# Performance work log

Hardware: AMD Instinct MI355X
Metric: run time of the kernel (lower is better)

Reference implementation:

```python
import jax, jax.numpy as jnp
import numpy as np

S, T, B = 32, 48, 1024      # src_len, tgt_len, batch
E, H = 256, 1024            # embedding, hidden
VS, VT = 256, 256           # source/target vocab


def setup_inputs() -> dict:
    key = jax.random.key(0)
    ks = jax.random.split(key, 20)
    s = 0.02
    n = jax.random.normal
    inp = {
        "src": jax.random.randint(ks[0], (S, B), 0, VS),
        "tgt": jax.random.randint(ks[1], (T, B), 0, VT),
        "enc_emb": n(ks[2], (VS, E), jnp.float32) * s,
        "enc_Wih0": n(ks[3], (4 * H, E), jnp.float32) * s,
        "enc_Whh0": n(ks[4], (4 * H, H), jnp.float32) * s,
        "enc_b0": jnp.zeros((4 * H,), jnp.float32),
        "enc_Wih1": n(ks[5], (4 * H, H), jnp.float32) * s,
        "enc_Whh1": n(ks[6], (4 * H, H), jnp.float32) * s,
        "enc_b1": jnp.zeros((4 * H,), jnp.float32),
        "dec_emb": n(ks[7], (VT, E), jnp.float32) * s,
        "dec_Wih0": n(ks[8], (4 * H, E), jnp.float32) * s,
        "dec_Whh0": n(ks[9], (4 * H, H), jnp.float32) * s,
        "dec_b0": jnp.zeros((4 * H,), jnp.float32),
        "dec_Wih1": n(ks[10], (4 * H, H), jnp.float32) * s,
        "dec_Whh1": n(ks[11], (4 * H, H), jnp.float32) * s,
        "dec_b1": jnp.zeros((4 * H,), jnp.float32),
        "fc_W": n(ks[12], (H, VT), jnp.float32) * s,
        "fc_b": jnp.zeros((VT,), jnp.float32),
    }
    return inp


def lstm_step(x, h, c, Wih, Whh, b):
    # PyTorch gate order: i, f, g, o
    z = x @ Wih.T + h @ Whh.T + b
    i, f, g, o = jnp.split(z, 4, axis=-1)
    c = jax.nn.sigmoid(f) * c + jax.nn.sigmoid(i) * jnp.tanh(g)
    h = jax.nn.sigmoid(o) * jnp.tanh(c)
    return h, c


def run_layer(xs, Wih, Whh, b):
    # xs: [S, B, in]; returns all hidden states and final (h, c)
    bsz = xs.shape[1]
    h0 = jnp.zeros((bsz, Whh.shape[1]), xs.dtype)

    def step(carry, x):
        h, c = lstm_step(x, carry[0], carry[1], Wih, Whh, b)
        return (h, c), h

    (h, c), hs = jax.lax.scan(step, (h0, h0), xs)
    return hs, h, c


def reference(src, tgt, enc_emb, enc_Wih0, enc_Whh0, enc_b0, enc_Wih1, enc_Whh1,
              enc_b1, dec_emb, dec_Wih0, dec_Whh0, dec_b0, dec_Wih1, dec_Whh1,
              dec_b1, fc_W, fc_b):
    # ---- Encoder: 2-layer LSTM over source ----
    xe = enc_emb[src]                                   # [S, B, E]
    hs0, h0, c0 = run_layer(xe, enc_Wih0, enc_Whh0, enc_b0)
    _, h1, c1 = run_layer(hs0, enc_Wih1, enc_Whh1, enc_b1)

    # ---- Decoder: per-timestep loop, teacher forcing ratio = 1.0 ----
    def dec_step(carry, tok):
        dh0, dc0, dh1, dc1 = carry
        x = dec_emb[tok]                                # [B, E]
        dh0, dc0 = lstm_step(x, dh0, dc0, dec_Wih0, dec_Whh0, dec_b0)
        dh1, dc1 = lstm_step(dh0, dh1, dc1, dec_Wih1, dec_Whh1, dec_b1)
        logits = dh1 @ fc_W + fc_b                      # [B, VT]
        return (dh0, dc0, dh1, dc1), logits

    _, logits = jax.lax.scan(dec_step, (h0, c0, h1, c1), tgt[:-1])  # [T-1, B, VT]
    # outputs[0] is never written in the original -> stays zeros
    out = jnp.concatenate([jnp.zeros((1,) + logits.shape[1:], logits.dtype), logits], axis=0)
    return out
```

## Files before the change

kernel.cpp:

```cpp
#include <hip/hip_runtime.h>
#include <hip/hip_fp16.h>

typedef __attribute__((ext_vector_type(8))) short short8;
typedef __attribute__((ext_vector_type(4))) float floatx4;

#define DEVFN static __device__ __forceinline__

DEVFN short f2h(float v) { return __half_as_short(__float2half(v)); }

DEVFN void gload16(const void* g, void* l) {
  void* gnc = const_cast<void*>(g);
  __builtin_amdgcn_global_load_lds(
      (__attribute__((address_space(1))) void*)gnc,
      (__attribute__((address_space(3))) void*)l, 16, 0, 0);
}

DEVFN unsigned* fset(unsigned* f, int role, int s, int gy) {
  return f + ((((role * 79) + s) * 8 + gy) << 5);
}

__global__ __launch_bounds__(256, 2) void pers_kernel(
    short* xe0, short* xe1, short* xd0, short* xd1,
    const short* wc_e0, const short* wc_e1, const short* wc_d0, const short* wc_d1,
    const float* eb0, const float* eb1, const float* db0, const float* db1,
    const short* embe, const short* embd,
    const int* __restrict__ src, const int* __restrict__ tgt,
    short* dh1, unsigned* flags) {
  __shared__ short smem[32768];
  const int tid = threadIdx.x;
  const int lane = tid & 63;
  const int wv = tid >> 6;
  const int wm = wv >> 1;
  const int wu = wv & 1;
  const int l15 = lane & 15;
  const int l4 = lane >> 4;
  const int bx = blockIdx.x;
  const int role1 = bx >> 5;
  const int ut = bx & 31;
  const int u0 = ut * 32;
  const int gy = blockIdx.y;
  const int m0 = gy * 128;
  const int srow = lane >> 3;
  const int swseg = ((lane & 7) * 16) ^ (srow * 16);
  const long SL0 = 1024l * 1280, SL1 = 1024l * 2048;

  float cst[16];
#pragma unroll
  for (int i = 0; i < 16; ++i) cst[i] = 0.f;

  for (int s = 0; s < 79; ++s) {
    unsigned* WA = nullptr;
    unsigned* WB = nullptr;
    if (!role1) {
      if (s >= 1) WA = fset(flags, 0, s - 1, gy);
      if (s >= 2) WB = fset(flags, 1, s - 2, gy);
    } else {
      WA = fset(flags, 0, s, gy);
      if (s >= 1) WB = fset(flags, 1, s - 1, gy);
    }
    if (WA || WB) {
      if (tid < 64) {
        unsigned* p = (tid < 32) ? (WA ? WA + tid : nullptr)
                                 : (WB ? WB + (tid - 32) : nullptr);
        if (p) {
          while (__hip_atomic_load(p, __ATOMIC_RELAXED,
                                   __HIP_MEMORY_SCOPE_AGENT) == 0u)
            __builtin_amdgcn_s_sleep(1);
          (void)__hip_atomic_load(p, __ATOMIC_ACQUIRE, __HIP_MEMORY_SCOPE_AGENT);
        }
      }
      __syncthreads();
    }

    const int enc = (s < 32) ? 1 : 0;
    const int t = enc ? s : s - 32;
    const int cur = t & 1, nxt = cur ^ 1;
    const short* A; const short* Wt; const float* bs; int ktot;
    short *d1 = nullptr, *d2 = nullptr, *d3 = nullptr, *xq = nullptr;
    int s1 = 0, o1 = 0, xs = 0;
    const short* xe = nullptr; const int* tk = nullptr;
    if (!role1) {
      if (enc) {
        A = xe0 + cur * SL0; Wt = wc_e0; bs = eb0; ktot = 1280;
        d2 = xe1 + cur * SL1;
        s1 = 1280; o1 = 256; xs = 1280;
        if (t < 31) { d1 = xe0 + nxt * SL0; xq = d1; xe = embe; tk = src + (t + 1) * 1024; }
        else        { d1 = xd0;             xq = xd0; xe = embd; tk = tgt; }
      } else {
        A = xd0 + cur * SL0; Wt = wc_d0; bs = db0; ktot = 1280;
        d1 = xd0 + nxt * SL0; s1 = 1280; o1 = 256;
        d2 = xd1 + cur * SL1;
        if (t < 46) { xq = xd0 + nxt * SL0; xs = 1280; xe = embd; tk = tgt + (t + 1) * 1024; }
      }
    } else {
      if (enc) {
        A = xe1 + cur * SL1; Wt = wc_e1; bs = eb1; ktot = 2048;
        d1 = (t < 31) ? (xe1 + nxt * SL1) : xd1; s1 = 2048; o1 = 1024;
      } else {
        A = xd1 + cur * SL1; Wt = wc_d1; bs = db1; ktot = 2048;
        d1 = xd1 + nxt * SL1; s1 = 2048; o1 = 1024;
        d3 = dh1 + (long)t * 1024 * 1024;
      }
    }

    floatx4 acc[4][4];
#pragma unroll
    for (int g = 0; g < 4; ++g)
#pragma unroll
      for (int mi = 0; mi < 4; ++mi) acc[g][mi] = (floatx4){0.f, 0.f, 0.f, 0.f};

    const char* Ab = (const char*)A;
    const char* Wb = (const char*)Wt;
    const long kbytes = (long)ktot * 2;
    const int nkb = ktot >> 6;

    auto stage = [&](int kb, int bufi) {
      const long kboff = (long)kb * 128;
      short* sb = smem + bufi * 16384;
#pragma unroll
      for (int ci = 0; ci < 8; ++ci) {
        const int c = wv * 8 + ci;
        void* lds = (void*)(sb + c * 512);
        if (c < 16) {
          const int row = c * 8 + srow;
          gload16(Ab + (long)(m0 + row) * kbytes + kboff + swseg, lds);
        } else {
          const int cb = c - 16;
          const int wrow = (cb >> 2) * 1024 + u0 + (cb & 3) * 8 + srow;
          gload16(Wb + (long)wrow * kbytes + kboff + swseg, lds);
        }
      }
    };

    stage(0, 0);
    __syncthreads();
    int buf = 0;
    for (int kb = 0; kb < nkb; ++kb) {
      if (kb + 1 < nkb) stage(kb + 1, buf ^ 1);
      const short* sb = smem + buf * 16384;
#pragma unroll
      for (int k0 = 0; k0 < 64; k0 += 32) {
        short8 fa[4];
        short8 fb[4];
#pragma unroll
        for (int mi = 0; mi < 4; ++mi) {
          const int r = wm * 64 + mi * 16 + l15;
          fa[mi] = *(const short8*)(sb + r * 64 + ((k0 + l4 * 8) ^ ((r & 7) << 3)));
        }
        {
          const int r = wu * 16 + l15;
          const int kk = (k0 + l4 * 8) ^ ((r & 7) << 3);
#pragma unroll
          for (int g = 0; g < 4; ++g)
            fb[g] = *(const short8*)(sb + 8192 + (g * 32 + r) * 64 + kk);
        }
#pragma unroll
        for (int g = 0; g < 4; ++g)
#pragma unroll
          for (int mi = 0; mi < 4; ++mi)
            asm volatile("v_mfma_f32_16x16x32_f16 %0, %1, %2, %0"
                         : "+v"(acc[g][mi])
                         : "v"(fa[mi]), "v"(fb[g]));
      }
      __syncthreads();
      buf ^= 1;
    }
    asm volatile("s_nop 7\ns_nop 7\ns_nop 7");

    const int u = u0 + wu * 16 + l15;
    const float bi = bs[u];
    const float bf_ = bs[1024 + u];
    const float bg = bs[2048 + u];
    const float bo = bs[3072 + u];
    short* ht = smem;
    const int uloc = wu * 16 + l15;
#pragma unroll
    for (int mi = 0; mi < 4; ++mi) {
#pragma unroll
      for (int j = 0; j < 4; ++j) {
        const float zi = acc[0][mi][j] + bi;
        const float zf = acc[1][mi][j] + bf_;
        const float zg = acc[2][mi][j] + bg;
        const float zo = acc[3][mi][j] + bo;
        const float gi = 1.f / (1.f + expf(-zi));
        const float gf = 1.f / (1.f + expf(-zf));
        const float gg = tanhf(zg);
        const float go = 1.f / (1.f + expf(-zo));
        const float cn = gf * cst[mi * 4 + j] + gi * gg;
        cst[mi * 4 + j] = cn;
        const int rl = wm * 64 + mi * 16 + l4 * 4 + j;
        ht[rl * 40 + uloc] = f2h(go * tanhf(cn));
      }
    }
    __syncthreads();

    {
      const int rl = tid >> 1;
      const int seg = (tid & 1) * 16;
      const short8 v0 = *(const short8*)(ht + rl * 40 + seg);
      const short8 v1 = *(const short8*)(ht + rl * 40 + seg + 8);
      const long col = u0 + seg;
      if (d1) {
        short* p = d1 + (long)(m0 + rl) * s1 + o1 + col;
        *(short8*)p = v0; *(short8*)(p + 8) = v1;
      }
      if (d2) {
        short* p = d2 + (long)(m0 + rl) * 2048 + col;
        *(short8*)p = v0; *(short8*)(p + 8) = v1;
      }
      if (d3) {
        short* p = d3 + (long)(m0 + rl) * 1024 + col;
        *(short8*)p = v0; *(short8*)(p + 8) = v1;
      }
    }
    if (xq && tid < 128) {
      const int i = ut * 128 + tid;
      const int row = i >> 5;
      const int e8 = (i & 31) * 8;
      const int b = m0 + row;
      const int tok = tk[b];
      const short8 v = *(const short8*)(xe + (long)tok * 256 + e8);
      *(short8*)(xq + (long)b * xs + e8) = v;
    }

    __syncthreads();
    if (tid == 0)
      __hip_atomic_store(fset(flags, role1, s, gy) + ut, 1u,
                         __ATOMIC_RELEASE, __HIP_MEMORY_SCOPE_AGENT);
  }
}

__global__ __launch_bounds__(256) void fc_kernel(
    const short* __restrict__ A, const short* __restrict__ W,
    const float* __restrict__ bias, float* __restrict__ outp) {
  __shared__ short smem[32768];
  const int tid = threadIdx.x;
  const int lane = tid & 63;
  const int wv = tid >> 6;
  const int wm = wv >> 1;
  const int wu = wv & 1;
  const int l15 = lane & 15;
  const int l4 = lane >> 4;
  const int u0 = blockIdx.x * 128;
  const int m0 = blockIdx.y * 128;
  const int srow = lane >> 3;
  const int swseg = ((lane & 7) * 16) ^ (srow * 16);

  floatx4 acc[4][4];
#pragma unroll
  for (int g = 0; g < 4; ++g)
#pragma unroll
    for (int mi = 0; mi < 4; ++mi) acc[g][mi] = (floatx4){0.f, 0.f, 0.f, 0.f};

  const char* Ab = (const char*)A;
  const char* Wb = (const char*)W;
  const long kbytes = 2048;
  const int nkb = 16;

  auto stage = [&](int kb, int bufi) {
    const long kboff = (long)kb * 128;
    short* sb = smem + bufi * 16384;
#pragma unroll
    for (int ci = 0; ci < 8; ++ci) {
      const int c = wv * 8 + ci;
      void* lds = (void*)(sb + c * 512);
      if (c < 16) {
        const int row = c * 8 + srow;
        gload16(Ab + (long)(m0 + row) * kbytes + kboff + swseg, lds);
      } else {
        const int cb = c - 16;
        const int wrow = (cb >> 2) * 32 + u0 + (cb & 3) * 8 + srow;
        gload16(Wb + (long)wrow * kbytes + kboff + swseg, lds);
      }
    }
  };

  stage(0, 0);
  __syncthreads();
  int buf = 0;
  for (int kb = 0; kb < nkb; ++kb) {
    if (kb + 1 < nkb) stage(kb + 1, buf ^ 1);
    const short* sb = smem + buf * 16384;
#pragma unroll
    for (int k0 = 0; k0 < 64; k0 += 32) {
      short8 fa[4];
      short8 fb[4];
#pragma unroll
      for (int mi = 0; mi < 4; ++mi) {
        const int r = wm * 64 + mi * 16 + l15;
        fa[mi] = *(const short8*)(sb + r * 64 + ((k0 + l4 * 8) ^ ((r & 7) << 3)));
      }
      {
        const int r = wu * 16 + l15;
        const int kk = (k0 + l4 * 8) ^ ((r & 7) << 3);
#pragma unroll
        for (int g = 0; g < 4; ++g)
          fb[g] = *(const short8*)(sb + 8192 + (g * 32 + r) * 64 + kk);
      }
#pragma unroll
      for (int g = 0; g < 4; ++g)
#pragma unroll
        for (int mi = 0; mi < 4; ++mi)
          asm volatile("v_mfma_f32_16x16x32_f16 %0, %1, %2, %0"
                       : "+v"(acc[g][mi])
                       : "v"(fa[mi]), "v"(fb[g]));
    }
    __syncthreads();
    buf ^= 1;
  }
  asm volatile("s_nop 7\ns_nop 7\ns_nop 7");

#pragma unroll
  for (int g = 0; g < 4; ++g) {
    const int n = u0 + g * 32 + wu * 16 + l15;
    const float bb = bias[n];
#pragma unroll
    for (int mi = 0; mi < 4; ++mi) {
#pragma unroll
      for (int j = 0; j < 4; ++j) {
        const int r = m0 + wm * 64 + mi * 16 + l4 * 4 + j;
        outp[(long)r * 256 + n] = acc[g][mi][j] + bb;
      }
    }
  }
}

__global__ void wprep(const float* __restrict__ A, const float* __restrict__ B,
                      short* __restrict__ dst, int N, int Ka, int Kb) {
  const int ktot = Ka + Kb;
  const int n8 = ktot >> 3;
  const int total = N * n8;
  for (int idx = blockIdx.x * 256 + threadIdx.x; idx < total; idx += gridDim.x * 256) {
    const int n = idx / n8;
    const int k = (idx - n * n8) * 8;
    const float* s = (k < Ka) ? (A + (long)n * Ka + k) : (B + (long)n * Kb + (k - Ka));
    short8 v;
#pragma unroll
    for (int j = 0; j < 8; ++j) v[j] = f2h(s[j]);
    *(short8*)(dst + (long)n * ktot + k) = v;
  }
}

__global__ void embprep(const float* __restrict__ s, short* __restrict__ d, int total8) {
  const int idx = blockIdx.x * 256 + threadIdx.x;
  if (idx >= total8) return;
  short8 v;
#pragma unroll
  for (int j = 0; j < 8; ++j) v[j] = f2h(s[idx * 8 + j]);
  *(short8*)(d + idx * 8) = v;
}

__global__ void fcwprep(const float* __restrict__ fcW, short* __restrict__ dst) {
  const int idx = blockIdx.x * 256 + threadIdx.x;
  const int v = idx & 255;
  const int h = (idx >> 8) * 8;
  short8 o;
#pragma unroll
  for (int j = 0; j < 8; ++j) o[j] = f2h(fcW[(long)(h + j) * 256 + v]);
  *(short8*)(dst + (long)v * 1024 + h) = o;
}

__global__ void initk(const int* __restrict__ src, const float* __restrict__ emb,
                      short* __restrict__ xe0, short* __restrict__ xe1) {
  const int idx = blockIdx.x * 256 + threadIdx.x;
  if (idx < 1024 * 160) {
    const int b = idx / 160;
    const int k = (idx - b * 160) * 8;
    short8 v;
    if (k < 256) {
      const int tok = src[b];
#pragma unroll
      for (int j = 0; j < 8; ++j) v[j] = f2h(emb[(long)tok * 256 + k + j]);
    } else {
#pragma unroll
      for (int j = 0; j < 8; ++j) v[j] = 0;
    }
    *(short8*)(xe0 + (long)b * 1280 + k) = v;
  } else {
    const int i = idx - 1024 * 160;
    if (i < 1024 * 128) {
      const int b = i >> 7;
      const int k = 1024 + (i & 127) * 8;
      short8 v;
#pragma unroll
      for (int j = 0; j < 8; ++j) v[j] = 0;
      *(short8*)(xe1 + (long)b * 2048 + k) = v;
    }
  }
}

extern "C" void kernel_launch(void* const* d_in, const int* in_sizes, int n_in,
                              void* d_out, int out_size, void* d_ws, size_t ws_size,
                              hipStream_t stream) {
  (void)in_sizes; (void)n_in; (void)out_size; (void)ws_size;
  const int* src = (const int*)d_in[0];
  const int* tgt = (const int*)d_in[1];
  const float* enc_emb = (const float*)d_in[2];
  const float* eW0i = (const float*)d_in[3];
  const float* eW0h = (const float*)d_in[4];
  const float* eb0 = (const float*)d_in[5];
  const float* eW1i = (const float*)d_in[6];
  const float* eW1h = (const float*)d_in[7];
  const float* eb1 = (const float*)d_in[8];
  const float* dec_emb = (const float*)d_in[9];
  const float* dW0i = (const float*)d_in[10];
  const float* dW0h = (const float*)d_in[11];
  const float* db0 = (const float*)d_in[12];
  const float* dW1i = (const float*)d_in[13];
  const float* dW1h = (const float*)d_in[14];
  const float* db1 = (const float*)d_in[15];
  const float* fcW = (const float*)d_in[16];
  const float* fcb = (const float*)d_in[17];
  float* out = (float*)d_out;

  char* ws = (char*)d_ws;
  size_t off = 0;
  auto carve = [&](size_t bytes) {
    void* p = ws + off;
    off += (bytes + 255) & ~(size_t)255;
    return p;
  };
  short* wc_e0 = (short*)carve(4096l * 1280 * 2);
  short* wc_e1 = (short*)carve(4096l * 2048 * 2);
  short* wc_d0 = (short*)carve(4096l * 1280 * 2);
  short* wc_d1 = (short*)carve(4096l * 2048 * 2);
  short* fcwt = (short*)carve(256l * 1024 * 2);
  short* embe = (short*)carve(256l * 256 * 2);
  short* embd = (short*)carve(256l * 256 * 2);
  short* xe0 = (short*)carve(2l * 1024 * 1280 * 2);
  short* xe1 = (short*)carve(2l * 1024 * 2048 * 2);
  short* xd0 = (short*)carve(2l * 1024 * 1280 * 2);
  short* xd1 = (short*)carve(2l * 1024 * 2048 * 2);
  short* dh1 = (short*)carve(47l * 1024 * 1024 * 2);
  const size_t flagbytes = 2l * 79 * 8 * 32 * 4;
  unsigned* flags = (unsigned*)carve(flagbytes);

  hipMemsetAsync(flags, 0, flagbytes, stream);
  hipMemsetAsync(out, 0, 1024l * 256 * 4, stream);

  wprep<<<2560, 256, 0, stream>>>(eW0i, eW0h, wc_e0, 4096, 256, 1024);
  wprep<<<4096, 256, 0, stream>>>(eW1i, eW1h, wc_e1, 4096, 1024, 1024);
  wprep<<<2560, 256, 0, stream>>>(dW0i, dW0h, wc_d0, 4096, 256, 1024);
  wprep<<<4096, 256, 0, stream>>>(dW1i, dW1h, wc_d1, 4096, 1024, 1024);
  embprep<<<32, 256, 0, stream>>>(enc_emb, embe, 8192);
  embprep<<<32, 256, 0, stream>>>(dec_emb, embd, 8192);
  fcwprep<<<128, 256, 0, stream>>>(fcW, fcwt);
  initk<<<1152, 256, 0, stream>>>(src, enc_emb, xe0, xe1);

  pers_kernel<<<dim3(64, 8), 256, 0, stream>>>(
      xe0, xe1, xd0, xd1, wc_e0, wc_e1, wc_d0, wc_d1,
      eb0, eb1, db0, db1, embe, embd, src, tgt, dh1, flags);

  fc_kernel<<<dim3(2, 376), 256, 0, stream>>>(dh1, fcwt, fcb, out + 1024l * 256);
}
```

Baseline: 4.210 ms.

## Deepen GEMM k-loop pipeline to 4-stage ring with k-tile of 32

Replaces the double-buffered 64-wide k-tile staging with a four-buffer ring of 32-wide k-tiles, keeping three tiles of global-to-LDS loads in flight via explicit vmcnt waits and a single barrier per iteration. The swizzle and row mapping are adjusted to the narrower tile. The aim is to hide global memory latency inside each recurrent step's GEMM. In exchange the loop runs twice as many iterations with one barrier each, so barrier and instruction overhead per MFMA rises.

```diff
diff --git a/kernel.cpp b/kernel.cpp
--- a/kernel.cpp
+++ b/kernel.cpp
@@ -40,8 +40,8 @@
   const int u0 = ut * 32;
   const int gy = blockIdx.y;
   const int m0 = gy * 128;
-  const int srow = lane >> 3;
-  const int swseg = ((lane & 7) * 16) ^ (srow * 16);
+  const int srow = lane >> 2;
+  const int sswz = ((lane & 3) * 16) ^ ((srow & 3) << 4);
   const long SL0 = 1024l * 1280, SL1 = 1024l * 2048;
 
   float cst[16];
@@ -112,59 +112,60 @@
     const char* Ab = (const char*)A;
     const char* Wb = (const char*)Wt;
     const long kbytes = (long)ktot * 2;
-    const int nkb = ktot >> 6;
+    const int nkb = ktot >> 5;
 
     auto stage = [&](int kb, int bufi) {
-      const long kboff = (long)kb * 128;
-      short* sb = smem + bufi * 16384;
-#pragma unroll
-      for (int ci = 0; ci < 8; ++ci) {
-        const int c = wv * 8 + ci;
-        void* lds = (void*)(sb + c * 512);
-        if (c < 16) {
-          const int row = c * 8 + srow;
-          gload16(Ab + (long)(m0 + row) * kbytes + kboff + swseg, lds);
+      const long kboff = (long)kb * 64;
+      short* sb = smem + bufi * 8192;
+#pragma unroll
+      for (int ci = 0; ci < 4; ++ci) {
+        const int c = wv * 4 + ci;
+        if (c < 8) {
+          const int row = m0 + c * 16 + srow;
+          gload16(Ab + (long)row * kbytes + kboff + sswz, sb + c * 512);
         } else {
-          const int cb = c - 16;
-          const int wrow = (cb >> 2) * 1024 + u0 + (cb & 3) * 8 + srow;
-          gload16(Wb + (long)wrow * kbytes + kboff + swseg, lds);
+          const int wr = (c - 8) * 16 + srow;
+          const int wrow = (wr >> 5) * 1024 + u0 + (wr & 31);
+          gload16(Wb + (long)wrow * kbytes + kboff + sswz, sb + 4096 + (c - 8) * 512);
         }
       }
     };
 
+    asm volatile("s_waitcnt vmcnt(0)" ::: "memory");
     stage(0, 0);
+    stage(1, 1);
+    stage(2, 2);
+    for (int kb = 0; kb < nkb; ++kb) {
+      if (kb + 2 < nkb)       asm volatile("s_waitcnt vmcnt(8)" ::: "memory");
+      else if (kb + 1 < nkb)  asm volatile("s_waitcnt vmcnt(4)" ::: "memory");
+      else                    asm volatile("s_waitcnt vmcnt(0)" ::: "memory");
+      __builtin_amdgcn_sched_barrier(0);
+      __builtin_amdgcn_s_barrier();
+      __builtin_amdgcn_sched_barrier(0);
+      if (kb + 3 < nkb) stage(kb + 3, (kb + 3) & 3);
+      __builtin_amdgcn_sched_barrier(0);
+      const short* sb = smem + (kb & 3) * 8192;
+      short8 fa[4];
+      short8 fb[4];
+#pragma unroll
+      for (int mi = 0; mi < 4; ++mi) {
+        const int r = wm * 64 + mi * 16 + l15;
+        fa[mi] = *(const short8*)(sb + r * 32 + ((l4 * 8) ^ ((r & 3) << 3)));
+      }
+#pragma unroll
+      for (int g = 0; g < 4; ++g) {
+        const int r = g * 32 + wu * 16 + l15;
+        fb[g] = *(const short8*)(sb + 4096 + r * 32 + ((l4 * 8) ^ ((r & 3) << 3)));
+      }
+#pragma unroll
+      for (int g = 0; g < 4; ++g)
+#pragma unroll
+        for (int mi = 0; mi < 4; ++mi)
+          asm volatile("v_mfma_f32_16x16x32_f16 %0, %1, %2, %0"
+                       : "+v"(acc[g][mi])
+                       : "v"(fa[mi]), "v"(fb[g]));
+    }
     __syncthreads();
-    int buf = 0;
-    for (int kb = 0; kb < nkb; ++kb) {
-      if (kb + 1 < nkb) stage(kb + 1, buf ^ 1);
-      const short* sb = smem + buf * 16384;
-#pragma unroll
-      for (int k0 = 0; k0 < 64; k0 += 32) {
-        short8 fa[4];
-        short8 fb[4];
-#pragma unroll
-        for (int mi = 0; mi < 4; ++mi) {
-          const int r = wm * 64 + mi * 16 + l15;
-          fa[mi] = *(const short8*)(sb + r * 64 + ((k0 + l4 * 8) ^ ((r & 7) << 3)));
-        }
-        {
-          const int r = wu * 16 + l15;
-          const int kk = (k0 + l4 * 8) ^ ((r & 7) << 3);
-#pragma unroll
-          for (int g = 0; g < 4; ++g)
-            fb[g] = *(const short8*)(sb + 8192 + (g * 32 + r) * 64 + kk);
-        }
-#pragma unroll
-        for (int g = 0; g < 4; ++g)
-#pragma unroll
-          for (int mi = 0; mi < 4; ++mi)
-            asm volatile("v_mfma_f32_16x16x32_f16 %0, %1, %2, %0"
-                         : "+v"(acc[g][mi])
-                         : "v"(fa[mi]), "v"(fb[g]));
-      }
-      __syncthreads();
-      buf ^= 1;
-    }
     asm volatile("s_nop 7\ns_nop 7\ns_nop 7");
 
     const int u = u0 + wu * 16 + l15;
```

New measurement: 5.035 ms. +19.6%, slower.
